# Kernel optimization log

Measured on AMD Instinct MI355X. Metric: run time of the kernel, lower is better.

Reference implementation:

```python
import jax, jax.numpy as jnp
import numpy as np

N = 50000      # nodes
E = 800000     # edges (avg degree 16)
EL = 200000    # link-prediction pairs
IN = 128       # in_channels
HID = 128      # hidden_conv_2


def setup_inputs() -> dict:
    key = jax.random.key(0)
    ks = jax.random.split(key, 12)
    x = jax.random.normal(ks[0], (N, IN), dtype=jnp.float32)
    edge_index = jax.random.randint(ks[1], (2, E), 0, N, dtype=jnp.int64)
    edge_label_index = jax.random.randint(ks[2], (2, EL), 0, N, dtype=jnp.int64)
    H = jnp.zeros((N, HID), dtype=jnp.float32)
    s_in = 1.0 / np.sqrt(IN)
    s_h = 1.0 / np.sqrt(HID)
    # Stacked ChebConv (K=2) weights for gates [z, r, h]:
    # Wx*: convs on the input x (IN -> HID); Wh*: convs on the state H (HID -> HID)
    Wx0 = jax.random.uniform(ks[3], (3, IN, HID), jnp.float32, -s_in, s_in)
    Wx1 = jax.random.uniform(ks[4], (3, IN, HID), jnp.float32, -s_in, s_in)
    bx = jax.random.uniform(ks[5], (3, HID), jnp.float32, -s_in, s_in)
    Wh0 = jax.random.uniform(ks[6], (3, HID, HID), jnp.float32, -s_h, s_h)
    Wh1 = jax.random.uniform(ks[7], (3, HID, HID), jnp.float32, -s_h, s_h)
    bh = jax.random.uniform(ks[8], (3, HID), jnp.float32, -s_h, s_h)
    post_w = jax.random.uniform(ks[9], (HID, 2), jnp.float32, -s_h, s_h)
    post_b = jax.random.uniform(ks[10], (2,), jnp.float32, -s_h, s_h)
    return {"x": x, "edge_index": edge_index, "edge_label_index": edge_label_index,
            "H": H, "Wx0": Wx0, "Wx1": Wx1, "bx": bx,
            "Wh0": Wh0, "Wh1": Wh1, "bh": bh,
            "post_w": post_w, "post_b": post_b}


def _gconv_gru(x, H, edge_index, Wx0, Wx1, bx, Wh0, Wh1, bh):
    src, dst = edge_index[0], edge_index[1]
    # Symmetric-normalized ChebConv edge weights with lambda_max=2:
    # L_hat = L - I = -D^{-1/2} A D^{-1/2}
    deg = jax.ops.segment_sum(jnp.ones(src.shape[0], x.dtype), src, num_segments=N)
    dinv = jnp.where(deg > 0, jax.lax.rsqrt(jnp.maximum(deg, 1e-12)), 0.0)
    norm = -(dinv[src] * dinv[dst])  # [E]

    def prop(v):  # L_hat @ v via gather-scale-scatter
        return jax.ops.segment_sum(v[src] * norm[:, None], dst, num_segments=N)

    px = prop(x)   # shared Tx_1 for all three x-convs
    pH = prop(H)

    def cheb_x(g):
        return x @ Wx0[g] + px @ Wx1[g] + bx[g]

    def cheb_h(v, pv, g):
        return v @ Wh0[g] + pv @ Wh1[g] + bh[g]

    Z = jax.nn.sigmoid(cheb_x(0) + cheb_h(H, pH, 0))
    R = jax.nn.sigmoid(cheb_x(1) + cheb_h(H, pH, 1))
    HR = H * R
    Ht = jnp.tanh(cheb_x(2) + cheb_h(HR, prop(HR), 2))
    return Z * H + (1.0 - Z) * Ht


def reference(x, edge_index, edge_label_index, H,
              Wx0, Wx1, bx, Wh0, Wh1, bh, post_w, post_b):
    h = _gconv_gru(x, H, edge_index, Wx0, Wx1, bx, Wh0, Wh1, bh)
    hidden = h  # detached copy in the original
    hr = jax.nn.relu(h)
    h_src = hr[edge_label_index[0]]  # [EL, HID]
    h_dst = hr[edge_label_index[1]]
    had = h_src * h_dst
    scores = jnp.sum(had @ post_w + post_b, axis=-1)  # [EL]
    return scores, hidden
```

## Files before the change

### kernel.cpp

```cpp
#include <hip/hip_runtime.h>

#define N_NODES 50000
#define N_EDGES 800000
#define N_EL    200000
#define CH      128

typedef __attribute__((ext_vector_type(8))) short bf16x8;
typedef __attribute__((ext_vector_type(4))) float f32x4;

__device__ __forceinline__ unsigned short f2bf(float f){
  unsigned int u = __float_as_uint(f);
  unsigned int r = (u + 0x7fff + ((u >> 16) & 1)) >> 16;
  return (unsigned short)r;
}
__device__ __forceinline__ float bflo(unsigned int v){ return __uint_as_float(v << 16); }
__device__ __forceinline__ float bfhi(unsigned int v){ return __uint_as_float(v & 0xffff0000u); }
__device__ __forceinline__ float bf2f(unsigned short u){ return __uint_as_float(((unsigned int)u) << 16); }

__global__ void hist_kernel(const int* __restrict__ ei, int* deg, int* cnt){
  int i = blockIdx.x*blockDim.x + threadIdx.x;
  if (i < N_EDGES){
    atomicAdd(&deg[ei[i]], 1);
    atomicAdd(&cnt[ei[N_EDGES + i]], 1);
  }
}

__global__ void dinv_kernel(const int* __restrict__ deg, float* __restrict__ dinv){
  int i = blockIdx.x*blockDim.x + threadIdx.x;
  if (i < N_NODES){
    int d = deg[i];
    dinv[i] = d > 0 ? rsqrtf((float)d) : 0.0f;
  }
}

#define SCAN_NB 196

__global__ void scan_bsum(const int* __restrict__ cnt, int* __restrict__ bsum){
  __shared__ int sh[256];
  int i = blockIdx.x*256 + threadIdx.x;
  sh[threadIdx.x] = (i < N_NODES) ? cnt[i] : 0;
  __syncthreads();
  for (int off = 128; off >= 1; off >>= 1){
    if ((int)threadIdx.x < off) sh[threadIdx.x] += sh[threadIdx.x + off];
    __syncthreads();
  }
  if (threadIdx.x == 0) bsum[blockIdx.x] = sh[0];
}

__global__ void scan_boff(const int* __restrict__ bsum, int* __restrict__ boff){
  __shared__ int sh[256];
  int t = threadIdx.x;
  int v = (t < SCAN_NB) ? bsum[t] : 0;
  sh[t] = v;
  __syncthreads();
  for (int off = 1; off < 256; off <<= 1){
    int tv = (t >= off) ? sh[t - off] : 0;
    __syncthreads();
    sh[t] += tv;
    __syncthreads();
  }
  if (t < SCAN_NB) boff[t] = sh[t] - v;
}

__global__ void scan_final(const int* __restrict__ cnt, const int* __restrict__ boff,
                           int* __restrict__ rowoff, int* __restrict__ cursor){
  __shared__ int sh[256];
  int t = threadIdx.x;
  int i = blockIdx.x*256 + t;
  int v = (i < N_NODES) ? cnt[i] : 0;
  sh[t] = v;
  __syncthreads();
  for (int off = 1; off < 256; off <<= 1){
    int tv = (t >= off) ? sh[t - off] : 0;
    __syncthreads();
    sh[t] += tv;
    __syncthreads();
  }
  int o = boff[blockIdx.x] + sh[t] - v;
  if (i < N_NODES){ rowoff[i] = o; cursor[i] = o; }
  if (i == N_NODES - 1) rowoff[N_NODES] = N_EDGES;
}

__global__ void scatter_kernel(const int* __restrict__ ei, const float* __restrict__ dinv,
                               int* cursor, int* __restrict__ csr_src,
                               float* __restrict__ csr_norm){
  int i = blockIdx.x*blockDim.x + threadIdx.x;
  if (i < N_EDGES){
    int s = ei[i];
    int d = ei[N_EDGES + i];
    int pos = atomicAdd(&cursor[d], 1);
    csr_src[pos]  = s;
    csr_norm[pos] = -(dinv[s] * dinv[d]);
  }
}

__global__ void cvt_xH(const float* __restrict__ x, const float* __restrict__ H,
                       unsigned short* __restrict__ xH){
  const int Q = (N_NODES*CH)/4;
  int i = blockIdx.x*blockDim.x + threadIdx.x;
  if (i >= 2*Q) return;
  const float* src = (i < Q) ? x : H;
  int off = (i < Q) ? i : i - Q;
  float4 v = ((const float4*)src)[off];
  int node = off >> 5, cg = off & 31;
  uint2 o;
  o.x = (unsigned int)f2bf(v.x) | ((unsigned int)f2bf(v.y) << 16);
  o.y = (unsigned int)f2bf(v.z) | ((unsigned int)f2bf(v.w) << 16);
  *(uint2*)(xH + (size_t)node*256 + ((i < Q) ? 0 : 128) + cg*4) = o;
}

__global__ void cvt_w(const float* __restrict__ Wx0, const float* __restrict__ Wx1,
                      const float* __restrict__ Wh0, const float* __restrict__ Wh1,
                      unsigned short* __restrict__ wt){
  int i = blockIdx.x*blockDim.x + threadIdx.x;
  if (i >= 12*128*128) return;
  int m = i >> 14;
  int r = i & 16383;
  int col = r >> 7, k = r & 127;
  const float* W[4] = {Wx0, Wx1, Wh0, Wh1};
  const float* src = W[m/3] + (m%3)*16384;
  wt[i] = f2bf(src[k*128 + col]);
}

__global__ void prop_x2(const int* __restrict__ rowoff, const int* __restrict__ csr_src,
                        const float* __restrict__ csr_norm,
                        const unsigned short* __restrict__ xH,
                        unsigned short* __restrict__ px, unsigned short* __restrict__ pH){
  int node = blockIdx.x*4 + ((int)threadIdx.x >> 6);
  if (node >= N_NODES) return;
  int lane = threadIdx.x & 63;
  int half = lane >> 5, il = lane & 31;
  const unsigned short* base = xH + half*128 + il*4;
  int beg = rowoff[node], end = rowoff[node+1];
  float a0 = 0.f, a1 = 0.f, a2 = 0.f, a3 = 0.f;
  int k = beg;
  for (; k + 4 <= end; k += 4){
    int s0 = csr_src[k], s1 = csr_src[k+1], s2 = csr_src[k+2], s3 = csr_src[k+3];
    float w0 = csr_norm[k], w1 = csr_norm[k+1], w2 = csr_norm[k+2], w3 = csr_norm[k+3];
    uint2 v0 = *(const uint2*)(base + (size_t)s0*256);
    uint2 v1 = *(const uint2*)(base + (size_t)s1*256);
    uint2 v2 = *(const uint2*)(base + (size_t)s2*256);
    uint2 v3 = *(const uint2*)(base + (size_t)s3*256);
    a0 += w0*bflo(v0.x) + w1*bflo(v1.x) + w2*bflo(v2.x) + w3*bflo(v3.x);
    a1 += w0*bfhi(v0.x) + w1*bfhi(v1.x) + w2*bfhi(v2.x) + w3*bfhi(v3.x);
    a2 += w0*bflo(v0.y) + w1*bflo(v1.y) + w2*bflo(v2.y) + w3*bflo(v3.y);
    a3 += w0*bfhi(v0.y) + w1*bfhi(v1.y) + w2*bfhi(v2.y) + w3*bfhi(v3.y);
  }
  for (; k < end; ++k){
    int s = csr_src[k];
    float w = csr_norm[k];
    uint2 v = *(const uint2*)(base + (size_t)s*256);
    a0 += w*bflo(v.x); a1 += w*bfhi(v.x);
    a2 += w*bflo(v.y); a3 += w*bfhi(v.y);
  }
  uint2 o;
  o.x = (unsigned int)f2bf(a0) | ((unsigned int)f2bf(a1) << 16);
  o.y = (unsigned int)f2bf(a2) | ((unsigned int)f2bf(a3) << 16);
  unsigned short* O = (half ? pH : px) + (size_t)node*CH + il*4;
  *(uint2*)O = o;
}

__global__ void prop_one(const int* __restrict__ rowoff, const int* __restrict__ csr_src,
                         const float* __restrict__ csr_norm,
                         const unsigned short* __restrict__ V,
                         unsigned short* __restrict__ O){
  int node = blockIdx.x*4 + ((int)threadIdx.x >> 6);
  if (node >= N_NODES) return;
  int lane = threadIdx.x & 63;
  const unsigned short* base = V + lane*2;
  int beg = rowoff[node], end = rowoff[node+1];
  float a0 = 0.f, a1 = 0.f;
  int k = beg;
  for (; k + 4 <= end; k += 4){
    int s0 = csr_src[k], s1 = csr_src[k+1], s2 = csr_src[k+2], s3 = csr_src[k+3];
    float w0 = csr_norm[k], w1 = csr_norm[k+1], w2 = csr_norm[k+2], w3 = csr_norm[k+3];
    unsigned int v0 = *(const unsigned int*)(base + (size_t)s0*256);
    unsigned int v1 = *(const unsigned int*)(base + (size_t)s1*256);
    unsigned int v2 = *(const unsigned int*)(base + (size_t)s2*256);
    unsigned int v3 = *(const unsigned int*)(base + (size_t)s3*256);
    a0 += w0*bflo(v0) + w1*bflo(v1) + w2*bflo(v2) + w3*bflo(v3);
    a1 += w0*bfhi(v0) + w1*bfhi(v1) + w2*bfhi(v2) + w3*bfhi(v3);
  }
  for (; k < end; ++k){
    int s = csr_src[k];
    float w = csr_norm[k];
    unsigned int v = *(const unsigned int*)(base + (size_t)s*256);
    a0 += w*bflo(v); a1 += w*bfhi(v);
  }
  *(unsigned int*)(O + (size_t)node*CH + lane*2) =
      (unsigned int)f2bf(a0) | ((unsigned int)f2bf(a1) << 16);
}

__launch_bounds__(256)
__global__ void mfma_gate01(const unsigned short* __restrict__ xH,
                            const unsigned short* __restrict__ px,
                            const unsigned short* __restrict__ pH,
                            const unsigned short* __restrict__ wt,
                            const float* __restrict__ bx, const float* __restrict__ bh,
                            unsigned short* __restrict__ zb,
                            unsigned short* __restrict__ xH_mut){
  const int M = 128*128;
  const unsigned short* Am[4] = {xH, px, xH + 128, pH};
  const int strA[4] = {256, 128, 256, 128};
  int lane = threadIdx.x & 63;
  int w    = threadIdx.x >> 6;
  int lr = lane & 15;
  int kb = (lane >> 4) * 8;
  int r0 = blockIdx.x * 128 + w * 32;

  f32x4 accZ[2][8], accR[2][8];
  #pragma unroll
  for (int i = 0; i < 2; ++i)
    #pragma unroll
    for (int c = 0; c < 8; ++c){
      accZ[i][c] = (f32x4){0.f,0.f,0.f,0.f};
      accR[i][c] = (f32x4){0.f,0.f,0.f,0.f};
    }

  int rA0 = min(r0 + lr,      N_NODES - 1);
  int rA1 = min(r0 + 16 + lr, N_NODES - 1);

  #pragma unroll
  for (int s = 0; s < 16; ++s){
    const int m = s >> 2;
    const int ko = (s & 3)*32 + kb;
    const unsigned short* Ap = Am[m] + ko;
    bf16x8 a0 = *(const bf16x8*)(Ap + (size_t)rA0*strA[m]);
    bf16x8 a1 = *(const bf16x8*)(Ap + (size_t)rA1*strA[m]);
    const unsigned short* Bz = wt + (size_t)(3*m + 0)*M + ko;
    const unsigned short* Br = wt + (size_t)(3*m + 1)*M + ko;
    #pragma unroll
    for (int c = 0; c < 8; ++c){
      bf16x8 bz = *(const bf16x8*)(Bz + (size_t)(c*16 + lr)*CH);
      bf16x8 br = *(const bf16x8*)(Br + (size_t)(c*16 + lr)*CH);
      accZ[0][c] = __builtin_amdgcn_mfma_f32_16x16x32_bf16(a0, bz, accZ[0][c], 0, 0, 0);
      accZ[1][c] = __builtin_amdgcn_mfma_f32_16x16x32_bf16(a1, bz, accZ[1][c], 0, 0, 0);
      accR[0][c] = __builtin_amdgcn_mfma_f32_16x16x32_bf16(a0, br, accR[0][c], 0, 0, 0);
      accR[1][c] = __builtin_amdgcn_mfma_f32_16x16x32_bf16(a1, br, accR[1][c], 0, 0, 0);
    }
  }

  float bsZ[8], bsR[8];
  #pragma unroll
  for (int c = 0; c < 8; ++c){
    bsZ[c] = bx[c*16 + lr]       + bh[c*16 + lr];
    bsR[c] = bx[128 + c*16 + lr] + bh[128 + c*16 + lr];
  }

  int rbase = r0 + (lane >> 4) * 4;
  #pragma unroll
  for (int i = 0; i < 2; ++i){
    #pragma unroll
    for (int j = 0; j < 4; ++j){
      int row = rbase + i*16 + j;
      if (row >= N_NODES) continue;
      size_t ro = (size_t)row * CH;
      size_t rh = (size_t)row * 256 + 128;
      #pragma unroll
      for (int c = 0; c < 8; ++c){
        int col = c*16 + lr;
        float z = 1.0f/(1.0f + __expf(-(accZ[i][c][j] + bsZ[c])));
        float r = 1.0f/(1.0f + __expf(-(accR[i][c][j] + bsR[c])));
        float h = bf2f(xH_mut[rh + col]);
        zb[ro + col]     = f2bf(z);
        xH_mut[rh + col] = f2bf(h * r);
      }
    }
  }
}

template<int EPI>
__launch_bounds__(256)
__global__ void mfma_gemm2(const unsigned short* __restrict__ A0, int sA0,
                           const unsigned short* __restrict__ A1, int sA1,
                           const unsigned short* __restrict__ B0,
                           const unsigned short* __restrict__ B1,
                           const float* __restrict__ bias,
                           const float* __restrict__ Hp, const float* __restrict__ pre2,
                           const unsigned short* __restrict__ zb,
                           float* __restrict__ out0f,
                           unsigned short* __restrict__ out1b){
  const unsigned short* Am[2] = {A0, A1};
  const int strA[2] = {sA0, sA1};
  const unsigned short* Bm[2] = {B0, B1};
  int lane = threadIdx.x & 63;
  int w    = threadIdx.x >> 6;
  int lr = lane & 15;
  int kb = (lane >> 4) * 8;
  int r0 = blockIdx.x * 128 + w * 32;

  f32x4 acc[2][8];
  #pragma unroll
  for (int i = 0; i < 2; ++i)
    #pragma unroll
    for (int c = 0; c < 8; ++c) acc[i][c] = (f32x4){0.f,0.f,0.f,0.f};

  int rA0 = min(r0 + lr,      N_NODES - 1);
  int rA1 = min(r0 + 16 + lr, N_NODES - 1);

  #pragma unroll
  for (int s = 0; s < 8; ++s){
    const int m = s >> 2;
    const int ko = (s & 3)*32 + kb;
    const unsigned short* Ap = Am[m] + ko;
    bf16x8 a0 = *(const bf16x8*)(Ap + (size_t)rA0*strA[m]);
    bf16x8 a1 = *(const bf16x8*)(Ap + (size_t)rA1*strA[m]);
    const unsigned short* Bp = Bm[m] + ko;
    #pragma unroll
    for (int c = 0; c < 8; ++c){
      bf16x8 b = *(const bf16x8*)(Bp + (size_t)(c*16 + lr)*CH);
      acc[0][c] = __builtin_amdgcn_mfma_f32_16x16x32_bf16(a0, b, acc[0][c], 0, 0, 0);
      acc[1][c] = __builtin_amdgcn_mfma_f32_16x16x32_bf16(a1, b, acc[1][c], 0, 0, 0);
    }
  }

  float bs[8];
  #pragma unroll
  for (int c = 0; c < 8; ++c) bs[c] = bias[c*16 + lr];

  int rbase = r0 + (lane >> 4) * 4;
  #pragma unroll
  for (int i = 0; i < 2; ++i){
    #pragma unroll
    for (int j = 0; j < 4; ++j){
      int row = rbase + i*16 + j;
      if (row >= N_NODES) continue;
      size_t ro = (size_t)row * CH;
      #pragma unroll
      for (int c = 0; c < 8; ++c){
        int col = c*16 + lr;
        size_t o = ro + col;
        float v = acc[i][c][j] + bs[c];
        if (EPI == 2){
          out0f[o] = v;
        } else {
          float ht = tanhf(v + pre2[o]);
          float z  = bf2f(zb[o]);
          float h  = z*Hp[o] + (1.0f - z)*ht;
          out0f[o] = h;
          out1b[o] = f2bf(fmaxf(h, 0.0f));
        }
      }
    }
  }
}

__global__ void scores_bf16(const int* __restrict__ eli, const unsigned short* __restrict__ hr,
                            const float* __restrict__ pw, const float* __restrict__ pb,
                            float* __restrict__ out){
  __shared__ float sw[CH];
  int t = threadIdx.x;
  if (t < CH) sw[t] = pw[2*t] + pw[2*t + 1];
  __syncthreads();
  int pair = blockIdx.x*16 + (t >> 4);
  if (pair >= N_EL) return;
  int il = t & 15;
  int a = eli[pair];
  int b = eli[N_EL + pair];
  bf16x8 va = *(const bf16x8*)(hr + (size_t)a*CH + il*8);
  bf16x8 vb = *(const bf16x8*)(hr + (size_t)b*CH + il*8);
  float s = 0.f;
  #pragma unroll
  for (int j = 0; j < 8; ++j){
    s += bf2f((unsigned short)va[j]) * bf2f((unsigned short)vb[j]) * sw[il*8 + j];
  }
  s += __shfl_xor(s, 1, 64);
  s += __shfl_xor(s, 2, 64);
  s += __shfl_xor(s, 4, 64);
  s += __shfl_xor(s, 8, 64);
  if (il == 0) out[pair] = s + pb[0] + pb[1];
}

extern "C" void kernel_launch(void* const* d_in, const int* in_sizes, int n_in,
                              void* d_out, int out_size, void* d_ws, size_t ws_size,
                              hipStream_t stream) {
  const float* x   = (const float*)d_in[0];
  const int*   ei  = (const int*)d_in[1];
  const int*   eli = (const int*)d_in[2];
  const float* H   = (const float*)d_in[3];
  const float* Wx0 = (const float*)d_in[4];
  const float* Wx1 = (const float*)d_in[5];
  const float* bx  = (const float*)d_in[6];
  const float* Wh0 = (const float*)d_in[7];
  const float* Wh1 = (const float*)d_in[8];
  const float* bh  = (const float*)d_in[9];
  const float* pw  = (const float*)d_in[10];
  const float* pb  = (const float*)d_in[11];
  float* out    = (float*)d_out;
  float* scores = out;
  float* hidden = out + N_EL;

  char* w = (char*)d_ws;
  auto alloc = [&](size_t b){ void* p = (void*)w; w += (b + 255) & ~(size_t)255; return p; };
  int*   deg      = (int*)  alloc((size_t)N_NODES*4);
  int*   cnt      = (int*)  alloc((size_t)N_NODES*4);
  float* dinv     = (float*)alloc((size_t)N_NODES*4);
  int*   rowoff   = (int*)  alloc((size_t)(N_NODES+1)*4);
  int*   cursor   = (int*)  alloc((size_t)N_NODES*4);
  int*   bsum     = (int*)  alloc((size_t)SCAN_NB*4);
  int*   boff     = (int*)  alloc((size_t)SCAN_NB*4);
  int*   csr_src  = (int*)  alloc((size_t)N_EDGES*4);
  float* csr_norm = (float*)alloc((size_t)N_EDGES*4);
  unsigned short* wt  = (unsigned short*)alloc((size_t)12*128*128*2);
  unsigned short* xHb = (unsigned short*)alloc((size_t)N_NODES*256*2);
  unsigned short* pxb = (unsigned short*)alloc((size_t)N_NODES*CH*2);
  unsigned short* pHb = (unsigned short*)alloc((size_t)N_NODES*CH*2);
  unsigned short* zbb = (unsigned short*)alloc((size_t)N_NODES*CH*2);
  float* pre2 = (float*)alloc((size_t)N_NODES*CH*4);
  unsigned short* pHRb   = pHb;
  unsigned short* relu_b = pxb;

  hipMemsetAsync(deg, 0, (size_t)N_NODES*4, stream);
  hipMemsetAsync(cnt, 0, (size_t)N_NODES*4, stream);

  hist_kernel<<<(N_EDGES+255)/256, 256, 0, stream>>>(ei, deg, cnt);
  dinv_kernel<<<(N_NODES+255)/256, 256, 0, stream>>>(deg, dinv);
  scan_bsum <<<SCAN_NB, 256, 0, stream>>>(cnt, bsum);
  scan_boff <<<1, 256, 0, stream>>>(bsum, boff);
  scan_final<<<SCAN_NB, 256, 0, stream>>>(cnt, boff, rowoff, cursor);
  scatter_kernel<<<(N_EDGES+255)/256, 256, 0, stream>>>(ei, dinv, cursor, csr_src, csr_norm);

  cvt_xH<<<(((N_NODES*CH)/4)*2 + 255)/256, 256, 0, stream>>>(x, H, xHb);
  cvt_w <<<(12*128*128 + 255)/256, 256, 0, stream>>>(Wx0, Wx1, Wh0, Wh1, wt);

  prop_x2<<<(N_NODES+3)/4, 256, 0, stream>>>(rowoff, csr_src, csr_norm, xHb, pxb, pHb);

  const int GB = (N_NODES + 127) / 128;
  const int M = 128*128;
  mfma_gate01<<<GB, 256, 0, stream>>>(xHb, pxb, pHb, wt, bx, bh, zbb, xHb);
  mfma_gemm2<2><<<GB, 256, 0, stream>>>(xHb, 256, pxb, 128,
      wt + (size_t)2*M, wt + (size_t)5*M, bx + 256,
      nullptr, nullptr, nullptr, pre2, nullptr);
  prop_one<<<(N_NODES+3)/4, 256, 0, stream>>>(rowoff, csr_src, csr_norm, xHb + 128, pHRb);
  mfma_gemm2<3><<<GB, 256, 0, stream>>>(xHb + 128, 256, pHRb, 128,
      wt + (size_t)8*M, wt + (size_t)11*M, bh + 256,
      H, pre2, zbb, hidden, relu_b);

  scores_bf16<<<(N_EL+15)/16, 256, 0, stream>>>(eli, relu_b, pw, pb, scores);
}
```

Before: 514.2 us.

## Fuse x-gate candidate GEMM into gate kernel and stage weights through LDS

Merges the separate pre2 (x-path candidate) GEMM into the z/r gate kernel so the A tiles of x and px are loaded once and reused for three outputs. Both MFMA kernels now stream weight tiles into swizzled, double-buffered LDS using global_load_lds instead of each wave reading B directly from global memory. The row tile shrinks from 128 to 64 rows per block, which doubles the grid and sets an occupancy hint of 3. The cost is extra barriers per k-step and higher register pressure from three accumulator sets.

Result: faster. 444.7 us (-13.5%).

```diff
diff --git a/kernel.cpp b/kernel.cpp
--- a/kernel.cpp
+++ b/kernel.cpp
@@ -16,6 +16,12 @@
 __device__ __forceinline__ float bflo(unsigned int v){ return __uint_as_float(v << 16); }
 __device__ __forceinline__ float bfhi(unsigned int v){ return __uint_as_float(v & 0xffff0000u); }
 __device__ __forceinline__ float bf2f(unsigned short u){ return __uint_as_float(((unsigned int)u) << 16); }
+
+__device__ __forceinline__ void gload16(const void* g, void* l){
+  __builtin_amdgcn_global_load_lds(
+      (const __attribute__((address_space(1))) unsigned int*)g,
+      (__attribute__((address_space(3))) unsigned int*)l, 16, 0, 0);
+}
 
 __global__ void hist_kernel(const int* __restrict__ ei, int* deg, int* cnt){
   int i = blockIdx.x*blockDim.x + threadIdx.x;
@@ -191,156 +197,170 @@
       (unsigned int)f2bf(a0) | ((unsigned int)f2bf(a1) << 16);
 }
 
-__launch_bounds__(256)
-__global__ void mfma_gate01(const unsigned short* __restrict__ xH,
-                            const unsigned short* __restrict__ px,
-                            const unsigned short* __restrict__ pH,
-                            const unsigned short* __restrict__ wt,
-                            const float* __restrict__ bx, const float* __restrict__ bh,
-                            unsigned short* __restrict__ zb,
-                            unsigned short* __restrict__ xH_mut){
+__launch_bounds__(256, 3)
+__global__ void mfma_gates(unsigned short* xH,
+                           const unsigned short* __restrict__ px,
+                           const unsigned short* __restrict__ pH,
+                           const unsigned short* __restrict__ wt,
+                           const float* __restrict__ bx, const float* __restrict__ bh,
+                           unsigned short* __restrict__ zb,
+                           float* __restrict__ pre2){
+  __shared__ unsigned short lds[2][3][4096];
   const int M = 128*128;
+  int lane = threadIdx.x & 63;
+  int w    = threadIdx.x >> 6;
+  int lr   = lane & 15;
+  int kq   = lane >> 4;
+  int r0w  = blockIdx.x*64 + w*16;
+  int rA   = min(r0w + lr, N_NODES - 1);
+
   const unsigned short* Am[4] = {xH, px, xH + 128, pH};
   const int strA[4] = {256, 128, 256, 128};
-  int lane = threadIdx.x & 63;
-  int w    = threadIdx.x >> 6;
-  int lr = lane & 15;
-  int kb = (lane >> 4) * 8;
-  int r0 = blockIdx.x * 128 + w * 32;
-
-  f32x4 accZ[2][8], accR[2][8];
-  #pragma unroll
-  for (int i = 0; i < 2; ++i)
+
+  const int scol = lane >> 2;
+  const int skbe = (((lane & 3) ^ ((lane >> 3) & 3)) << 3);
+  auto stage = [&](int s, int b){
+    int t = s >> 2, ko = (s & 3) * 32;
+    int nm = (t < 2) ? 3 : 2;
+    for (int q = w; q < nm*8; q += 4){
+      int g = q >> 3, i = q & 7;
+      const unsigned short* src = wt + (size_t)(t*3 + g)*M
+                                + (size_t)(i*16 + scol)*CH + ko + skbe;
+      gload16(src, &lds[b][g][i*512]);
+    }
+  };
+
+  f32x4 accZ[8], accR[8], accP[8];
+  #pragma unroll
+  for (int c = 0; c < 8; ++c){
+    accZ[c] = (f32x4){0.f,0.f,0.f,0.f};
+    accR[c] = (f32x4){0.f,0.f,0.f,0.f};
+    accP[c] = (f32x4){0.f,0.f,0.f,0.f};
+  }
+
+  const int rdo = ((kq ^ ((lr >> 1) & 3)) << 3);
+
+  stage(0, 0);
+  __syncthreads();
+  #pragma unroll
+  for (int s = 0; s < 16; ++s){
+    const int b = s & 1;
+    if (s < 15) stage(s + 1, b ^ 1);
+    const int t = s >> 2, ko = (s & 3) * 32;
+    bf16x8 a = *(const bf16x8*)(Am[t] + (size_t)rA*strA[t] + ko + kq*8);
     #pragma unroll
     for (int c = 0; c < 8; ++c){
-      accZ[i][c] = (f32x4){0.f,0.f,0.f,0.f};
-      accR[i][c] = (f32x4){0.f,0.f,0.f,0.f};
-    }
-
-  int rA0 = min(r0 + lr,      N_NODES - 1);
-  int rA1 = min(r0 + 16 + lr, N_NODES - 1);
-
-  #pragma unroll
-  for (int s = 0; s < 16; ++s){
-    const int m = s >> 2;
-    const int ko = (s & 3)*32 + kb;
-    const unsigned short* Ap = Am[m] + ko;
-    bf16x8 a0 = *(const bf16x8*)(Ap + (size_t)rA0*strA[m]);
-    bf16x8 a1 = *(const bf16x8*)(Ap + (size_t)rA1*strA[m]);
-    const unsigned short* Bz = wt + (size_t)(3*m + 0)*M + ko;
-    const unsigned short* Br = wt + (size_t)(3*m + 1)*M + ko;
+      bf16x8 bz = *(const bf16x8*)&lds[b][0][(c*16 + lr)*32 + rdo];
+      bf16x8 br = *(const bf16x8*)&lds[b][1][(c*16 + lr)*32 + rdo];
+      accZ[c] = __builtin_amdgcn_mfma_f32_16x16x32_bf16(a, bz, accZ[c], 0, 0, 0);
+      accR[c] = __builtin_amdgcn_mfma_f32_16x16x32_bf16(a, br, accR[c], 0, 0, 0);
+      if (t < 2){
+        bf16x8 bp = *(const bf16x8*)&lds[b][2][(c*16 + lr)*32 + rdo];
+        accP[c] = __builtin_amdgcn_mfma_f32_16x16x32_bf16(a, bp, accP[c], 0, 0, 0);
+      }
+    }
+    __syncthreads();
+  }
+
+  float bsZ[8], bsR[8], bsP[8];
+  #pragma unroll
+  for (int c = 0; c < 8; ++c){
+    int col = c*16 + lr;
+    bsZ[c] = bx[col]       + bh[col];
+    bsR[c] = bx[128 + col] + bh[128 + col];
+    bsP[c] = bx[256 + col];
+  }
+
+  #pragma unroll
+  for (int j = 0; j < 4; ++j){
+    int row = r0w + kq*4 + j;
+    if (row >= N_NODES) continue;
+    size_t ro = (size_t)row * CH;
+    size_t rh = (size_t)row * 256 + 128;
     #pragma unroll
     for (int c = 0; c < 8; ++c){
-      bf16x8 bz = *(const bf16x8*)(Bz + (size_t)(c*16 + lr)*CH);
-      bf16x8 br = *(const bf16x8*)(Br + (size_t)(c*16 + lr)*CH);
-      accZ[0][c] = __builtin_amdgcn_mfma_f32_16x16x32_bf16(a0, bz, accZ[0][c], 0, 0, 0);
-      accZ[1][c] = __builtin_amdgcn_mfma_f32_16x16x32_bf16(a1, bz, accZ[1][c], 0, 0, 0);
-      accR[0][c] = __builtin_amdgcn_mfma_f32_16x16x32_bf16(a0, br, accR[0][c], 0, 0, 0);
-      accR[1][c] = __builtin_amdgcn_mfma_f32_16x16x32_bf16(a1, br, accR[1][c], 0, 0, 0);
-    }
-  }
-
-  float bsZ[8], bsR[8];
-  #pragma unroll
-  for (int c = 0; c < 8; ++c){
-    bsZ[c] = bx[c*16 + lr]       + bh[c*16 + lr];
-    bsR[c] = bx[128 + c*16 + lr] + bh[128 + c*16 + lr];
-  }
-
-  int rbase = r0 + (lane >> 4) * 4;
-  #pragma unroll
-  for (int i = 0; i < 2; ++i){
-    #pragma unroll
-    for (int j = 0; j < 4; ++j){
-      int row = rbase + i*16 + j;
-      if (row >= N_NODES) continue;
-      size_t ro = (size_t)row * CH;
-      size_t rh = (size_t)row * 256 + 128;
-      #pragma unroll
-      for (int c = 0; c < 8; ++c){
-        int col = c*16 + lr;
-        float z = 1.0f/(1.0f + __expf(-(accZ[i][c][j] + bsZ[c])));
-        float r = 1.0f/(1.0f + __expf(-(accR[i][c][j] + bsR[c])));
-        float h = bf2f(xH_mut[rh + col]);
-        zb[ro + col]     = f2bf(z);
-        xH_mut[rh + col] = f2bf(h * r);
-      }
-    }
-  }
-}
-
-template<int EPI>
-__launch_bounds__(256)
-__global__ void mfma_gemm2(const unsigned short* __restrict__ A0, int sA0,
-                           const unsigned short* __restrict__ A1, int sA1,
+      int col = c*16 + lr;
+      float z = 1.0f/(1.0f + __expf(-(accZ[c][j] + bsZ[c])));
+      float r = 1.0f/(1.0f + __expf(-(accR[c][j] + bsR[c])));
+      float h = bf2f(xH[rh + col]);
+      zb[ro + col]   = f2bf(z);
+      xH[rh + col]   = f2bf(h * r);
+      pre2[ro + col] = accP[c][j] + bsP[c];
+    }
+  }
+}
+
+__launch_bounds__(256, 3)
+__global__ void mfma_final(const unsigned short* __restrict__ hr,
+                           const unsigned short* __restrict__ phr,
                            const unsigned short* __restrict__ B0,
                            const unsigned short* __restrict__ B1,
                            const float* __restrict__ bias,
                            const float* __restrict__ Hp, const float* __restrict__ pre2,
                            const unsigned short* __restrict__ zb,
-                           float* __restrict__ out0f,
-                           unsigned short* __restrict__ out1b){
-  const unsigned short* Am[2] = {A0, A1};
-  const int strA[2] = {sA0, sA1};
-  const unsigned short* Bm[2] = {B0, B1};
+                           float* __restrict__ hidden,
+                           unsigned short* __restrict__ relu_b){
+  __shared__ unsigned short lds[2][4096];
   int lane = threadIdx.x & 63;
   int w    = threadIdx.x >> 6;
-  int lr = lane & 15;
-  int kb = (lane >> 4) * 8;
-  int r0 = blockIdx.x * 128 + w * 32;
-
-  f32x4 acc[2][8];
-  #pragma unroll
-  for (int i = 0; i < 2; ++i)
-    #pragma unroll
-    for (int c = 0; c < 8; ++c) acc[i][c] = (f32x4){0.f,0.f,0.f,0.f};
-
-  int rA0 = min(r0 + lr,      N_NODES - 1);
-  int rA1 = min(r0 + 16 + lr, N_NODES - 1);
-
+  int lr   = lane & 15;
+  int kq   = lane >> 4;
+  int r0w  = blockIdx.x*64 + w*16;
+  int rA   = min(r0w + lr, N_NODES - 1);
+
+  const unsigned short* Am[2] = {hr, phr};
+  const int strA[2] = {256, 128};
+
+  const int scol = lane >> 2;
+  const int skbe = (((lane & 3) ^ ((lane >> 3) & 3)) << 3);
+  auto stage = [&](int s, int b){
+    int t = s >> 2, ko = (s & 3) * 32;
+    const unsigned short* B = t ? B1 : B0;
+    for (int q = w; q < 8; q += 4){
+      const unsigned short* src = B + (size_t)(q*16 + scol)*CH + ko + skbe;
+      gload16(src, &lds[b][q*512]);
+    }
+  };
+
+  f32x4 acc[8];
+  #pragma unroll
+  for (int c = 0; c < 8; ++c) acc[c] = (f32x4){0.f,0.f,0.f,0.f};
+
+  const int rdo = ((kq ^ ((lr >> 1) & 3)) << 3);
+
+  stage(0, 0);
+  __syncthreads();
   #pragma unroll
   for (int s = 0; s < 8; ++s){
-    const int m = s >> 2;
-    const int ko = (s & 3)*32 + kb;
-    const unsigned short* Ap = Am[m] + ko;
-    bf16x8 a0 = *(const bf16x8*)(Ap + (size_t)rA0*strA[m]);
-    bf16x8 a1 = *(const bf16x8*)(Ap + (size_t)rA1*strA[m]);
-    const unsigned short* Bp = Bm[m] + ko;
+    const int b = s & 1;
+    if (s < 7) stage(s + 1, b ^ 1);
+    const int t = s >> 2, ko = (s & 3) * 32;
+    bf16x8 a = *(const bf16x8*)(Am[t] + (size_t)rA*strA[t] + ko + kq*8);
     #pragma unroll
     for (int c = 0; c < 8; ++c){
-      bf16x8 b = *(const bf16x8*)(Bp + (size_t)(c*16 + lr)*CH);
-      acc[0][c] = __builtin_amdgcn_mfma_f32_16x16x32_bf16(a0, b, acc[0][c], 0, 0, 0);
-      acc[1][c] = __builtin_amdgcn_mfma_f32_16x16x32_bf16(a1, b, acc[1][c], 0, 0, 0);
-    }
+      bf16x8 bb = *(const bf16x8*)&lds[b][(c*16 + lr)*32 + rdo];
+      acc[c] = __builtin_amdgcn_mfma_f32_16x16x32_bf16(a, bb, acc[c], 0, 0, 0);
+    }
+    __syncthreads();
   }
 
   float bs[8];
   #pragma unroll
   for (int c = 0; c < 8; ++c) bs[c] = bias[c*16 + lr];
 
-  int rbase = r0 + (lane >> 4) * 4;
-  #pragma unroll
-  for (int i = 0; i < 2; ++i){
+  #pragma unroll
+  for (int j = 0; j < 4; ++j){
+    int row = r0w + kq*4 + j;
+    if (row >= N_NODES) continue;
+    size_t ro = (size_t)row * CH;
     #pragma unroll
-    for (int j = 0; j < 4; ++j){
-      int row = rbase + i*16 + j;
-      if (row >= N_NODES) continue;
-      size_t ro = (size_t)row * CH;
-      #pragma unroll
-      for (int c = 0; c < 8; ++c){
-        int col = c*16 + lr;
-        size_t o = ro + col;
-        float v = acc[i][c][j] + bs[c];
-        if (EPI == 2){
-          out0f[o] = v;
-        } else {
-          float ht = tanhf(v + pre2[o]);
-          float z  = bf2f(zb[o]);
-          float h  = z*Hp[o] + (1.0f - z)*ht;
-          out0f[o] = h;
-          out1b[o] = f2bf(fmaxf(h, 0.0f));
-        }
-      }
+    for (int c = 0; c < 8; ++c){
+      size_t o = ro + c*16 + lr;
+      float ht = tanhf(acc[c][j] + bs[c] + pre2[o]);
+      float z  = bf2f(zb[o]);
+      float h  = z*Hp[o] + (1.0f - z)*ht;
+      hidden[o] = h;
+      relu_b[o] = f2bf(fmaxf(h, 0.0f));
     }
   }
 }
@@ -425,16 +445,12 @@
 
   prop_x2<<<(N_NODES+3)/4, 256, 0, stream>>>(rowoff, csr_src, csr_norm, xHb, pxb, pHb);
 
-  const int GB = (N_NODES + 127) / 128;
-  const int M = 128*128;
-  mfma_gate01<<<GB, 256, 0, stream>>>(xHb, pxb, pHb, wt, bx, bh, zbb, xHb);
-  mfma_gemm2<2><<<GB, 256, 0, stream>>>(xHb, 256, pxb, 128,
-      wt + (size_t)2*M, wt + (size_t)5*M, bx + 256,
-      nullptr, nullptr, nullptr, pre2, nullptr);
+  const int GB = (N_NODES + 63) / 64;
+  const size_t M = 128*128;
+  mfma_gates<<<GB, 256, 0, stream>>>(xHb, pxb, pHb, wt, bx, bh, zbb, pre2);
   prop_one<<<(N_NODES+3)/4, 256, 0, stream>>>(rowoff, csr_src, csr_norm, xHb + 128, pHRb);
-  mfma_gemm2<3><<<GB, 256, 0, stream>>>(xHb + 128, 256, pHRb, 128,
-      wt + (size_t)8*M, wt + (size_t)11*M, bh + 256,
-      H, pre2, zbb, hidden, relu_b);
+  mfma_final<<<GB, 256, 0, stream>>>(xHb + 128, pHRb, wt + 8*M, wt + 11*M,
+      bh + 256, H, pre2, zbb, hidden, relu_b);
 
   scores_bf16<<<(N_EL+15)/16, 256, 0, stream>>>(eli, relu_b, pw, pb, scores);
 }
```
